# Kernel optimization log

Hardware: AMD Instinct MI355X
Metric: run time of the kernel (lower is better)

The kernel has to match this reference:

```python
import jax, jax.numpy as jnp
import numpy as np

LATENT = 256
HEADS = 4
DIM_HEAD = 256            # dim_head = latent_channels
INNER = HEADS * DIM_HEAD  # 1024
ROT_DIM = DIM_HEAD // 2   # rotary dim per coordinate (relative_emb_dim=2)
MIN_FREQ = 1.0 / 64.0     # 1/res
ROT_SCALE = 16.0          # CrossFormer scale
FF_SCALE = 0.5            # Gaussian Fourier feature scale
PI = 3.141592653589793
OUT_CH = 3


def _gelu(x):
    return jax.nn.gelu(x, approximate=False)  # torch nn.GELU default (erf)


def _rot_freqs(coords, dim):
    # coords: [b, n] -> freqs [b, n, dim]
    inv_freq = 1.0 / (10000.0 ** (jnp.arange(0, dim, 2, dtype=jnp.float32) / dim))
    t = coords * (ROT_SCALE / MIN_FREQ)
    f = t[..., None] * inv_freq               # [b, n, dim//2]
    return jnp.concatenate([f, f], axis=-1)    # [b, n, dim]


def _rotate_half(x):
    x1, x2 = jnp.split(x, 2, axis=-1)
    return jnp.concatenate([-x2, x1], axis=-1)


def _apply_rot(t, freqs):
    return t * jnp.cos(freqs) + _rotate_half(t) * jnp.sin(freqs)


def _apply_2d_rot(t, fx, fy):
    d = t.shape[-1]
    tx, ty = t[..., : d // 2], t[..., d // 2 :]
    return jnp.concatenate([_apply_rot(tx, fx), _apply_rot(ty, fy)], axis=-1)


def _inst_norm(t, eps=1e-5):
    # galerkin normalization: non-affine norm over head dim (InstanceNorm1d, affine=False)
    mu = jnp.mean(t, axis=-1, keepdims=True)
    var = jnp.var(t, axis=-1, keepdims=True)
    return (t - mu) * jax.lax.rsqrt(var + eps)


def setup_inputs() -> dict:
    key = jax.random.key(0)
    ks = jax.random.split(key, 20)
    b, nq, nc = 8, 4096, 4096
    s = 0.02
    return {
        "z": jax.random.normal(ks[0], (b, nc, LATENT), jnp.float32),
        "query_pos": jax.random.uniform(ks[1], (b, nq, 2), jnp.float32),
        "context_pos": jax.random.uniform(ks[2], (b, nc, 2), jnp.float32),
        # GaussianFourierFeatureTransform buffer B: [2, mapping_size=latent/2]
        "B_ff": jax.random.normal(ks[3], (2, LATENT // 2), jnp.float32) * FF_SCALE,
        # coordinate_projection linears (bias=False)
        "Wc1": jax.random.normal(ks[4], (LATENT, LATENT), jnp.float32) * s,
        "Wc2": jax.random.normal(ks[5], (LATENT, LATENT), jnp.float32) * s,
        # cross attention projections
        "Wq": jax.random.normal(ks[6], (LATENT, INNER), jnp.float32) * s,
        "Wkv": jax.random.normal(ks[7], (LATENT, 2 * INNER), jnp.float32) * s,
        "Wo": jax.random.normal(ks[8], (INNER, LATENT), jnp.float32) * s,
        "bo": jnp.zeros((LATENT,), jnp.float32),
        # feed-forward (mlp_dim = latent)
        "Wf1": jax.random.normal(ks[9], (LATENT, LATENT), jnp.float32) * s,
        "bf1": jnp.zeros((LATENT,), jnp.float32),
        "Wf2": jax.random.normal(ks[10], (LATENT, LATENT), jnp.float32) * s,
        "bf2": jnp.zeros((LATENT,), jnp.float32),
        # output head
        "Wh1": jax.random.normal(ks[11], (LATENT + 2, LATENT), jnp.float32) * s,
        "Wh2": jax.random.normal(ks[12], (LATENT, LATENT // 2), jnp.float32) * s,
        "Wh3": jax.random.normal(ks[13], (LATENT // 2, OUT_CH), jnp.float32) * s,
        "bh3": jnp.zeros((OUT_CH,), jnp.float32),
    }


def reference(z, query_pos, context_pos, B_ff, Wc1, Wc2, Wq, Wkv, Wo, bo,
              Wf1, bf1, Wf2, bf2, Wh1, Wh2, Wh3, bh3):
    b, nq, _ = query_pos.shape
    nc = z.shape[1]
    # 1) Gaussian Fourier features + 2-layer projection
    ff = 2.0 * PI * (query_pos @ B_ff)                           # [b, nq, latent/2]
    x = jnp.concatenate([jnp.sin(ff), jnp.cos(ff)], axis=-1)      # [b, nq, latent]
    x = _gelu(x @ Wc1) @ Wc2
    # 2) galerkin cross attention with 2D rotary relative pos emb
    q = (x @ Wq).reshape(b, nq, HEADS, DIM_HEAD).transpose(0, 2, 1, 3)
    k, v = jnp.split(z @ Wkv, 2, axis=-1)
    k = k.reshape(b, nc, HEADS, DIM_HEAD).transpose(0, 2, 1, 3)
    v = v.reshape(b, nc, HEADS, DIM_HEAD).transpose(0, 2, 1, 3)
    fxq = _rot_freqs(query_pos[..., 0], ROT_DIM)[:, None]         # [b,1,nq,rot]
    fyq = _rot_freqs(query_pos[..., 1], ROT_DIM)[:, None]
    fxk = _rot_freqs(context_pos[..., 0], ROT_DIM)[:, None]
    fyk = _rot_freqs(context_pos[..., 1], ROT_DIM)[:, None]
    q = _apply_2d_rot(q, fxq, fyq)
    k = _apply_2d_rot(k, fxk, fyk)
    k = _inst_norm(k)
    v = _inst_norm(v)
    kv = jnp.einsum('bhnd,bhne->bhde', k, v)                      # [b,h,d,d]
    attn = jnp.einsum('bhmd,bhde->bhme', q, kv) * (1.0 / nc)      # [b,h,nq,d]
    attn = attn.transpose(0, 2, 1, 3).reshape(b, nq, INNER)
    x = (attn @ Wo + bo) + x                                      # residual
    x = (_gelu(x @ Wf1 + bf1) @ Wf2 + bf2) + x                    # FFN residual
    # 3) output head on [features, coords]
    h = jnp.concatenate([x, query_pos], axis=-1)
    h = _gelu(h @ Wh1)
    h = _gelu(h @ Wh2)
    return h @ Wh3 + bh3                                          # [b, nq, out_ch]
```

## Files before the change

kernel.cpp:

```cpp
#include <hip/hip_runtime.h>
#include <math.h>


typedef unsigned short u16;
typedef __attribute__((ext_vector_type(4))) float f32x4;
typedef __attribute__((ext_vector_type(8))) short s16x8;
typedef __attribute__((ext_vector_type(8))) unsigned short u16x8;
typedef __attribute__((ext_vector_type(4))) unsigned short u16x4;

#define LOG2_1E4_D64 0.20762050593046013f

__device__ __forceinline__ u16 f2b(float f){
  union { float f; unsigned u; } v; v.f = f;
  unsigned u = v.u;
  u += 0x7FFFu + ((u >> 16) & 1u);
  return (u16)(u >> 16);
}
__device__ __forceinline__ float b2f(u16 b){
  union { unsigned u; float f; } v; v.u = ((unsigned)b) << 16; return v.f;
}
__device__ __forceinline__ float gelu_f(float x){
  return 0.5f * x * (1.0f + erff(x * 0.7071067811865475f));
}

#if __has_builtin(__builtin_amdgcn_global_load_lds)
#define HAVE_GLL 1
typedef const __attribute__((address_space(1))) void* as1cv;
typedef __attribute__((address_space(3))) void* as3v;
__device__ __forceinline__ void gload16(const void* g, void* l){
  __builtin_amdgcn_global_load_lds((as1cv)g, (as3v)l, 16, 0, 0);
}
#else
#define HAVE_GLL 0
#endif


__global__ __launch_bounds__(256) void k_cast(const float* __restrict__ in, u16* __restrict__ out){
  long i = (long)blockIdx.x * 256 + threadIdx.x;
  float4 f = ((const float4*)in)[i];
  u16x4 o = { f2b(f.x), f2b(f.y), f2b(f.z), f2b(f.w) };
  ((u16x4*)out)[i] = o;
}

struct TCArgs {
  const float* W[9]; u16* Wt[9];
  int K[9]; int N[9]; int boff[10];
};
__global__ __launch_bounds__(256) void k_tcast_all(TCArgs a){
  int b = blockIdx.x;
  int w = 0;
  while (b >= a.boff[w+1]) w++;
  int idx = (b - a.boff[w]) * 256 + threadIdx.x;
  int K = a.K[w], N = a.N[w];
  int n = idx / K, k = idx - n * K;
  a.Wt[w][idx] = f2b(a.W[w][(long)k * N + n]);
}

__global__ __launch_bounds__(256) void k_fourier(const float* __restrict__ qp, const float* __restrict__ Bff, u16* __restrict__ X0){
  int tid = threadIdx.x;
  long r = (long)blockIdx.x * 2 + (tid >> 7);
  int j = tid & 127;
  float qx = qp[r*2], qy = qp[r*2+1];
  float ff = 6.283185307179586f * (qx * Bff[j] + qy * Bff[128 + j]);
  X0[r*256 + j]       = f2b(sinf(ff));
  X0[r*256 + 128 + j] = f2b(cosf(ff));
}

__global__ __launch_bounds__(256) void k_red(const float* __restrict__ p, u16* __restrict__ out, long stride){
  long i = (long)blockIdx.x * 256 + threadIdx.x;
  f32x4 s = ((const f32x4*)p)[i];
  s += ((const f32x4*)(p + stride))[i];
  s += ((const f32x4*)(p + 2*stride))[i];
  s += ((const f32x4*)(p + 3*stride))[i];
  u16x4 o = { f2b(s[0]), f2b(s[1]), f2b(s[2]), f2b(s[3]) };
  ((u16x4*)out)[i] = o;
}

__global__ __launch_bounds__(256) void k_final(const u16* __restrict__ H2, const float* __restrict__ Wh3,
                                               const float* __restrict__ bh3, float* __restrict__ out){
  long r = (long)blockIdx.x * 256 + threadIdx.x;
  float a0 = bh3[0], a1 = bh3[1], a2 = bh3[2];
  const u16x8* hrow = (const u16x8*)(H2 + r*128);
#pragma unroll
  for (int c8 = 0; c8 < 16; c8++){
    u16x8 hv = hrow[c8];
#pragma unroll
    for (int e = 0; e < 8; e++){
      float f = b2f(hv[e]);
      int k = c8*8 + e;
      a0 += f * Wh3[k*3];
      a1 += f * Wh3[k*3+1];
      a2 += f * Wh3[k*3+2];
    }
  }
  out[r*3] = a0; out[r*3+1] = a1; out[r*3+2] = a2;
}


template<int MODE>
__global__ __launch_bounds__(256, 2)
void gemm_fuse(const u16* __restrict__ A, const u16* __restrict__ Bw,
               u16* __restrict__ out, const float* __restrict__ pos){
  __shared__ u16 As[128*32];
  __shared__ u16 Bs[256*32];

  int tid  = threadIdx.x;
  int lane = tid & 63;
  int wave = tid >> 6;
  int wm = (wave & 1) << 6;
  int wn = (wave >> 1) << 7;
  int whalf = wave >> 1;
  int h = blockIdx.y;
  long m0 = (long)blockIdx.x * 128;

  int r15 = lane & 15;
  int cc  = lane >> 4;
  const u16* Bh = Bw + (long)h * 65536;

#if HAVE_GLL
  int srow = lane >> 2;
  int scol = (lane & 3) * 8;
  u16* lA[2]; const u16* gA[2];
#pragma unroll
  for (int t = 0; t < 2; t++){
    int rb = (wave*2 + t) * 16;
    lA[t] = &As[rb*32];
    gA[t] = A + (m0 + rb + srow) * 256 + scol;
  }
  u16* lB[4]; const u16* gB[4];
#pragma unroll
  for (int t = 0; t < 4; t++){
    int rb = (wave*4 + t) * 16;
    lB[t] = &Bs[rb*32];
    gB[t] = Bh + (rb + srow) * 256 + scol;
  }
#else
  int sm  = tid >> 2;
  int sc  = tid & 3;
#endif

  f32x4 acc[4][8];
#pragma unroll
  for (int i = 0; i < 4; i++)
#pragma unroll
    for (int j = 0; j < 8; j++)
      acc[i][j] = f32x4{0.f, 0.f, 0.f, 0.f};

  for (int k0 = 0; k0 < 256; k0 += 32){
#if HAVE_GLL
    __syncthreads();
#pragma unroll
    for (int t = 0; t < 2; t++) gload16(gA[t] + k0, lA[t]);
#pragma unroll
    for (int t = 0; t < 4; t++) gload16(gB[t] + k0, lB[t]);
    __syncthreads();
#else
    u16x8 va = *(const u16x8*)(A + (m0 + sm)*256 + sc*8 + k0);
    u16x8 vb0 = *(const u16x8*)(Bh + (sm      )*256 + sc*8 + k0);
    u16x8 vb1 = *(const u16x8*)(Bh + (sm + 64 )*256 + sc*8 + k0);
    u16x8 vb2 = *(const u16x8*)(Bh + (sm + 128)*256 + sc*8 + k0);
    u16x8 vb3 = *(const u16x8*)(Bh + (sm + 192)*256 + sc*8 + k0);
    u16x8 va1 = *(const u16x8*)(A + (m0 + sm + 64)*256 + sc*8 + k0);
    __syncthreads();
    *(u16x8*)&As[sm*32 + sc*8] = va;
    *(u16x8*)&As[(sm+64)*32 + sc*8] = va1;
    *(u16x8*)&Bs[sm*32 + sc*8] = vb0;
    *(u16x8*)&Bs[(sm+64)*32 + sc*8] = vb1;
    *(u16x8*)&Bs[(sm+128)*32 + sc*8] = vb2;
    *(u16x8*)&Bs[(sm+192)*32 + sc*8] = vb3;
    __syncthreads();
#endif
    s16x8 af[4], bf[8];
#pragma unroll
    for (int i = 0; i < 4; i++) af[i] = *(const s16x8*)&As[(wm + i*16 + r15)*32 + cc*8];
#pragma unroll
    for (int j = 0; j < 8; j++) bf[j] = *(const s16x8*)&Bs[(wn + j*16 + r15)*32 + cc*8];
#pragma unroll
    for (int i = 0; i < 4; i++)
#pragma unroll
      for (int j = 0; j < 8; j++)
        acc[i][j] = __builtin_amdgcn_mfma_f32_16x16x32_bf16(af[i], bf[j], acc[i][j], 0, 0, 0);
  }

  if constexpr (MODE != 1){
    float invf4[4];
#pragma unroll
    for (int jl = 0; jl < 4; jl++)
      invf4[jl] = 1024.0f * exp2f(-(float)(jl*16 + r15) * LOG2_1E4_D64);
#pragma unroll
    for (int i = 0; i < 4; i++){
#pragma unroll
      for (int r = 0; r < 4; r++){
        long n = m0 + wm + i*16 + cc*4 + r;
        float p = pos[n*2 + whalf];
#pragma unroll
        for (int jl = 0; jl < 4; jl++){
          float a = p * invf4[jl];
          float s = __sinf(a), c = __cosf(a);
          float t0 = acc[i][jl][r], t1 = acc[i][jl+4][r];
          acc[i][jl][r]   = t0*c - t1*s;
          acc[i][jl+4][r] = t1*c + t0*s;
        }
      }
    }
  }

  if constexpr (MODE == 2){
#pragma unroll
    for (int i = 0; i < 4; i++)
#pragma unroll
      for (int j = 0; j < 8; j++)
#pragma unroll
        for (int r = 0; r < 4; r++){
          long row = m0 + wm + i*16 + cc*4 + r;
          int col = h*256 + wn + j*16 + r15;
          out[row*1024 + col] = f2b(acc[i][j][r]);
        }
  } else {
    __shared__ float PS1[2][128];
    __shared__ float PS2[2][128];
    __shared__ u16 TB[64*256];

    float s1a[4][4], s2a[4][4];
#pragma unroll
    for (int i = 0; i < 4; i++){
#pragma unroll
      for (int r = 0; r < 4; r++){
        float s1 = 0.f, s2 = 0.f;
#pragma unroll
        for (int j = 0; j < 8; j++){
          float v = acc[i][j][r];
          s1 += v; s2 += v*v;
        }
#pragma unroll
        for (int m = 1; m < 16; m <<= 1){
          s1 += __shfl_xor(s1, m, 64);
          s2 += __shfl_xor(s2, m, 64);
        }
        s1a[i][r] = s1; s2a[i][r] = s2;
        int rowid = (wave&1)*64 + i*16 + cc*4 + r;
        if (r15 == 0){ PS1[whalf][rowid] = s1; PS2[whalf][rowid] = s2; }
      }
    }
    __syncthreads();
#pragma unroll
    for (int i = 0; i < 4; i++){
#pragma unroll
      for (int r = 0; r < 4; r++){
        int rowid = (wave&1)*64 + i*16 + cc*4 + r;
        float s1 = PS1[0][rowid] + PS1[1][rowid];
        float s2 = PS2[0][rowid] + PS2[1][rowid];
        float mu  = s1 * 0.00390625f;
        float var = s2 * 0.00390625f - mu*mu;
        float inv = 1.0f / sqrtf(var + 1e-5f);
#pragma unroll
        for (int j = 0; j < 8; j++)
          acc[i][j] = f32x4{ (acc[i][j][0+0]-0.f), acc[i][j][1], acc[i][j][2], acc[i][j][3] },
          acc[i][j][r] = (acc[i][j][r] - mu) * inv;
      }
    }
    __syncthreads();

    int bb  = (int)(m0 >> 12);
    int nn0 = (int)(m0 & 4095);
    long matbase = ((long)(bb*4 + h) * 256) * 4096;
#pragma unroll
    for (int p = 0; p < 2; p++){
      if ((wave & 1) == p){
#pragma unroll
        for (int i = 0; i < 4; i++)
#pragma unroll
          for (int j = 0; j < 8; j++)
#pragma unroll
            for (int r = 0; r < 4; r++){
              int nl = i*16 + cc*4 + r;
              int d  = wn + j*16 + r15;
              TB[nl*256 + (d ^ ((nl>>2)<<1))] = f2b(acc[i][j][r]);
            }
      }
      __syncthreads();
      {
        int n4 = (lane & 15) * 4;
        int sw = (lane & 15) << 1;
#pragma unroll
        for (int rnd = 0; rnd < 16; rnd++){
          int d = rnd*16 + wave*4 + (lane >> 4);
          u16x4 vv;
#pragma unroll
          for (int jj = 0; jj < 4; jj++) vv[jj] = TB[(n4+jj)*256 + (d ^ sw)];
          *(u16x4*)(out + matbase + (long)d*4096 + nn0 + p*64 + n4) = vv;
        }
      }
      __syncthreads();
    }
  }
}


enum { EP_B = 0, EP_GELU = 1, EP_BIAS_GELU = 2, EP_BIAS_RESB = 3, EP_SCALE = 4,
       EP_QP_GELU = 5, EP_F32 = 6 };

struct GArgs {
  const u16* A; const u16* B;
  u16* Cb; float* Cf;
  const float* bias; const u16* res; const float* qp; const float* wtail;
  float scale;
  int M, N, K, lda, ldb, ldc, NLO;
  long sAh, sAl, sBh, sBl, sCh, sCl;
};

template<int EP>
__global__ __launch_bounds__(256, 2)
void gemm_k(GArgs g){
  int z = blockIdx.z;
  int zh = z / g.NLO, zl = z - zh * g.NLO;
  const u16* A = g.A + (long)zh * g.sAh + (long)zl * g.sAl;
  const u16* B = g.B + (long)zh * g.sBh + (long)zl * g.sBl;
  long coff = (long)zh * g.sCh + (long)zl * g.sCl;

  __shared__ u16 As[128*32];
  __shared__ u16 Bs[128*32];

  int tid  = threadIdx.x;
  int lane = tid & 63;
  int wave = tid >> 6;
  int wm = (wave & 1) << 6;
  int wn = (wave >> 1) << 6;
  long m0 = (long)blockIdx.x * 128;
  long n0 = (long)blockIdx.y * 128;

  int r15 = lane & 15;
  int cc  = lane >> 4;

#if HAVE_GLL
  int rA0 = (wave*2 + 0) * 16;
  int rA1 = (wave*2 + 1) * 16;
  int srow = lane >> 2;
  int scol = (lane & 3) * 8;
  u16* lA0 = &As[rA0*32];
  u16* lA1 = &As[rA1*32];
  u16* lB0 = &Bs[rA0*32];
  u16* lB1 = &Bs[rA1*32];
  const u16* gA0 = A + (m0 + rA0 + srow) * g.lda + scol;
  const u16* gA1 = A + (m0 + rA1 + srow) * g.lda + scol;
  const u16* gB0 = B + (n0 + rA0 + srow) * g.ldb + scol;
  const u16* gB1 = B + (n0 + rA1 + srow) * g.ldb + scol;
#else
  int sm  = tid >> 2;
  int sc  = tid & 3;
  int so0 = sm * 32 + sc * 8;
  int so1 = (sm + 64) * 32 + sc * 8;
  const u16* pA0 = A + (m0 + sm ) * g.lda + sc * 8;
  const u16* pA1 = A + (m0 + sm + 64) * g.lda + sc * 8;
  const u16* pB0 = B + (n0 + sm ) * g.ldb + sc * 8;
  const u16* pB1 = B + (n0 + sm + 64) * g.ldb + sc * 8;
#endif

  f32x4 acc[4][4];
#pragma unroll
  for (int i = 0; i < 4; i++)
#pragma unroll
    for (int j = 0; j < 4; j++)
      acc[i][j] = f32x4{0.f, 0.f, 0.f, 0.f};

  for (int k0 = 0; k0 < g.K; k0 += 32){
#if HAVE_GLL
    __syncthreads();
    gload16(gA0 + k0, lA0);
    gload16(gA1 + k0, lA1);
    gload16(gB0 + k0, lB0);
    gload16(gB1 + k0, lB1);
    __syncthreads();
#else
    u16x8 va0 = *(const u16x8*)(pA0 + k0);
    u16x8 va1 = *(const u16x8*)(pA1 + k0);
    u16x8 vb0 = *(const u16x8*)(pB0 + k0);
    u16x8 vb1 = *(const u16x8*)(pB1 + k0);
    __syncthreads();
    *(u16x8*)&As[so0] = va0;
    *(u16x8*)&As[so1] = va1;
    *(u16x8*)&Bs[so0] = vb0;
    *(u16x8*)&Bs[so1] = vb1;
    __syncthreads();
#endif
    s16x8 af[4], bf[4];
#pragma unroll
    for (int i = 0; i < 4; i++) af[i] = *(const s16x8*)&As[(wm + i*16 + r15)*32 + cc*8];
#pragma unroll
    for (int i = 0; i < 4; i++) bf[i] = *(const s16x8*)&Bs[(wn + i*16 + r15)*32 + cc*8];
#pragma unroll
    for (int i = 0; i < 4; i++)
#pragma unroll
      for (int j = 0; j < 4; j++)
        acc[i][j] = __builtin_amdgcn_mfma_f32_16x16x32_bf16(af[i], bf[j], acc[i][j], 0, 0, 0);
  }

  int colb = (int)n0 + wn + r15;
  int rowb = (int)m0 + wm + cc * 4;
#pragma unroll
  for (int i = 0; i < 4; i++){
#pragma unroll
    for (int j = 0; j < 4; j++){
      int col = colb + j*16;
#pragma unroll
      for (int r = 0; r < 4; r++){
        int row = rowb + i*16 + r;
        float v = acc[i][j][r];
        if constexpr (EP == EP_B){
          g.Cb[coff + (long)row * g.ldc + col] = f2b(v);
        } else if constexpr (EP == EP_GELU){
          g.Cb[coff + (long)row * g.ldc + col] = f2b(gelu_f(v));
        } else if constexpr (EP == EP_BIAS_GELU){
          v = gelu_f(v + g.bias[col]);
          g.Cb[coff + (long)row * g.ldc + col] = f2b(v);
        } else if constexpr (EP == EP_BIAS_RESB){
          v += g.bias[col] + b2f(g.res[(long)row * g.ldc + col]);
          g.Cb[coff + (long)row * g.ldc + col] = f2b(v);
        } else if constexpr (EP == EP_SCALE){
          g.Cb[coff + (long)row * g.ldc + col] = f2b(v * g.scale);
        } else if constexpr (EP == EP_F32){
          g.Cf[coff + (long)row * g.ldc + col] = v;
        } else {
          v += g.qp[(long)row*2] * g.wtail[col] + g.qp[(long)row*2+1] * g.wtail[256+col];
          g.Cb[coff + (long)row * g.ldc + col] = f2b(gelu_f(v));
        }
      }
    }
  }
}


extern "C" void kernel_launch(void* const* d_in, const int* in_sizes, int n_in,
                              void* d_out, int out_size, void* d_ws, size_t ws_size,
                              hipStream_t stream){
  const float* z   = (const float*)d_in[0];
  const float* qp  = (const float*)d_in[1];
  const float* cp  = (const float*)d_in[2];
  const float* Bff = (const float*)d_in[3];
  const float* Wc1 = (const float*)d_in[4];
  const float* Wc2 = (const float*)d_in[5];
  const float* Wq  = (const float*)d_in[6];
  const float* Wkv = (const float*)d_in[7];
  const float* Wo  = (const float*)d_in[8];
  const float* bo  = (const float*)d_in[9];
  const float* Wf1 = (const float*)d_in[10];
  const float* bf1 = (const float*)d_in[11];
  const float* Wf2 = (const float*)d_in[12];
  const float* bf2 = (const float*)d_in[13];
  const float* Wh1 = (const float*)d_in[14];
  const float* Wh2 = (const float*)d_in[15];
  const float* Wh3 = (const float*)d_in[16];
  const float* bh3 = (const float*)d_in[17];
  float* out = (float*)d_out;
  (void)in_sizes; (void)n_in; (void)out_size;

  size_t mb = ws_size >> 20;
  int C;
  if      (mb >= 264) C = 1;
  else if (mb >= 168) C = 2;
  else if (mb >= 120) C = 4;
  else                C = 8;
  const int NB = 8 / C;
  const long R = (long)NB * 4096;

  char* ws = (char*)d_ws;
  const size_t MB = 1024*1024;
  u16* WqT  = (u16*)(ws + 0);
  u16* WkvT = (u16*)(ws + 512*1024);
  u16* WoT  = (u16*)(ws + 1536*1024);
  u16* Wc1T = (u16*)(ws + 2048*1024);
  u16* Wc2T = (u16*)(ws + (2048+128)*1024);
  u16* Wf1T = (u16*)(ws + (2048+256)*1024);
  u16* Wf2T = (u16*)(ws + (2048+384)*1024);
  u16* Wh1T = (u16*)(ws + (2048+512)*1024);
  u16* Wh2T = (u16*)(ws + (2048+640)*1024);
  u16* R1 = (u16*)(ws + 4*MB);
  u16* R2 = (u16*)(ws + 20*MB);
  u16* R3 = (u16*)(ws + 36*MB);
  u16* R4 = (u16*)(ws + 52*MB);
  u16* kvT = (u16*)(ws + 68*MB);
  u16* BIG1 = (u16*)(ws + 72*MB);
  u16* BIG2 = (u16*)((char*)BIG1 + (size_t)NB*8*MB);
  u16* BIG3 = (u16*)((char*)BIG2 + (size_t)NB*8*MB);

  u16* X0b = R1; u16* X2b = R1;
  u16* Tb  = R2; u16* H1b = R2;
  u16* Xb  = R3;
  u16* Zb  = R4; u16* H2b = R4;

  auto G = [&](int ep, const u16* A, const u16* B, u16* Cb, float* Cf,
               const float* bias, const u16* res, const float* qq, const float* wtail,
               float scale, int M, int N, int K, int lda, int ldb, int ldc,
               int nz, int NLO, long sAh, long sAl, long sBh, long sBl, long sCh, long sCl){
    GArgs g;
    g.A=A; g.B=B; g.Cb=Cb; g.Cf=Cf; g.bias=bias; g.res=res; g.qp=qq; g.wtail=wtail;
    g.scale=scale; g.M=M; g.N=N; g.K=K; g.lda=lda; g.ldb=ldb; g.ldc=ldc; g.NLO=NLO;
    g.sAh=sAh; g.sAl=sAl; g.sBh=sBh; g.sBl=sBl; g.sCh=sCh; g.sCl=sCl;
    dim3 gr(M/128, N/128, nz); dim3 bl(256);
    switch(ep){
      case EP_B:          gemm_k<EP_B><<<gr,bl,0,stream>>>(g); break;
      case EP_GELU:       gemm_k<EP_GELU><<<gr,bl,0,stream>>>(g); break;
      case EP_BIAS_GELU:  gemm_k<EP_BIAS_GELU><<<gr,bl,0,stream>>>(g); break;
      case EP_BIAS_RESB:  gemm_k<EP_BIAS_RESB><<<gr,bl,0,stream>>>(g); break;
      case EP_SCALE:      gemm_k<EP_SCALE><<<gr,bl,0,stream>>>(g); break;
      case EP_QP_GELU:    gemm_k<EP_QP_GELU><<<gr,bl,0,stream>>>(g); break;
      case EP_F32:        gemm_k<EP_F32><<<gr,bl,0,stream>>>(g); break;
    }
  };

  k_cast<<<dim3(8192), dim3(256), 0, stream>>>(z, Zb);
  {
    TCArgs a;
    const float* Ws[9] = { Wq, Wkv, Wo, Wc1, Wc2, Wf1, Wf2, Wh1, Wh2 };
    u16* Wts[9] = { WqT, WkvT, WoT, Wc1T, Wc2T, Wf1T, Wf2T, Wh1T, Wh2T };
    int Ks[9] = { 256, 256, 1024, 256, 256, 256, 256, 256, 256 };
    int Ns[9] = { 1024, 2048, 256, 256, 256, 256, 256, 256, 128 };
    int off = 0;
    for (int i = 0; i < 9; i++){
      a.W[i] = Ws[i]; a.Wt[i] = Wts[i]; a.K[i] = Ks[i]; a.N[i] = Ns[i];
      a.boff[i] = off; off += Ks[i]*Ns[i]/256;
    }
    a.boff[9] = off;
    k_tcast_all<<<dim3(off), dim3(256), 0, stream>>>(a);
  }

  k_fourier<<<dim3(16384), dim3(256), 0, stream>>>(qp, Bff, X0b);
  G(EP_GELU, X0b, Wc1T, Tb, 0, 0,0,0,0, 1.f, 32768,256,256, 256,256,256, 1,1, 0,0,0,0,0,0);
  G(EP_B,    Tb,  Wc2T, Xb, 0, 0,0,0,0, 1.f, 32768,256,256, 256,256,256, 1,1, 0,0,0,0,0,0);

  for (int c = 0; c < C; c++){
    long row0 = (long)c * R;
    const u16* Zc = Zb + row0 * 256;
    gemm_fuse<0><<<dim3((int)(R/128), 4), dim3(256), 0, stream>>>(Zc, WkvT, BIG2, cp + row0*2);
    gemm_fuse<1><<<dim3((int)(R/128), 4), dim3(256), 0, stream>>>(Zc, WkvT + 1024*256, BIG3, cp + row0*2);
    G(EP_F32, BIG3, BIG2, 0, (float*)BIG1, 0,0,0,0, 1.f,
      256,256,1024, 4096,4096,256, 4*NB*4, NB*4,
      1024,1048576, 1024,1048576, (long)NB*4*65536,65536);
    k_red<<<dim3(NB*256), dim3(256), 0, stream>>>((float*)BIG1, kvT + (long)c*NB*4*65536, (long)NB*4*65536);
    gemm_fuse<2><<<dim3((int)(R/128), 4), dim3(256), 0, stream>>>(Xb + row0*256, WqT, BIG1, qp + row0*2);
    G(EP_SCALE, BIG1, kvT + (long)c*NB*4*65536, BIG2, 0, 0,0,0,0, 1.0f/4096.0f,
      4096,256,256, 1024,256,1024, NB*4,4, 4194304,256, 262144,65536, 4194304,256);
    G(EP_BIAS_RESB, BIG2, WoT, X2b + row0*256, 0, bo, Xb + row0*256, 0,0, 1.f,
      (int)R,256,1024, 1024,1024,256, 1,1, 0,0,0,0,0,0);
  }

  G(EP_BIAS_GELU, X2b, Wf1T, Tb, 0, bf1, 0,0,0, 1.f, 32768,256,256, 256,256,256, 1,1, 0,0,0,0,0,0);
  G(EP_BIAS_RESB, Tb, Wf2T, Xb, 0, bf2, X2b, 0,0, 1.f, 32768,256,256, 256,256,256, 1,1, 0,0,0,0,0,0);
  G(EP_QP_GELU, Xb, Wh1T, H1b, 0, 0,0, qp, Wh1 + 65536, 1.f, 32768,256,256, 256,256,256, 1,1, 0,0,0,0,0,0);
  G(EP_GELU, H1b, Wh2T, H2b, 0, 0,0,0,0, 1.f, 32768,128,256, 256,256,128, 1,1, 0,0,0,0,0,0);
  k_final<<<dim3(128), dim3(256), 0, stream>>>(H2b, Wh3, bh3, out);
}
```

Before: 603.1 us.

## Double-buffer LDS tiles in GEMMs and merge K/V projection launches

Both the fused projection kernel and the generic GEMM now double-buffer their shared-memory tiles, prefetching the next K-slice with global-to-LDS loads while MFMAs run on the current one, which removes one barrier per iteration. The separate K and V projection launches are merged into one launch with 8 column blocks, using a block-index check to pick rotary and output target. The grid is reordered so column blocks vary fastest, for A-tile reuse in cache. Shared memory is reused through one 48KB buffer, which may limit occupancy, and the non-GLL fallback was rewritten awkwardly.

```diff
diff --git a/kernel.cpp b/kernel.cpp
--- a/kernel.cpp
+++ b/kernel.cpp
@@ -100,9 +100,11 @@
 template<int MODE>
 __global__ __launch_bounds__(256, 2)
 void gemm_fuse(const u16* __restrict__ A, const u16* __restrict__ Bw,
-               u16* __restrict__ out, const float* __restrict__ pos){
-  __shared__ u16 As[128*32];
-  __shared__ u16 Bs[256*32];
+               u16* __restrict__ outK, u16* __restrict__ outV,
+               const float* __restrict__ pos){
+  __shared__ char smem[49152];
+  u16* AsB[2] = { (u16*)smem,            (u16*)(smem + 8192)  };
+  u16* BsB[2] = { (u16*)(smem + 16384),  (u16*)(smem + 32768) };
 
   int tid  = threadIdx.x;
   int lane = tid & 63;
@@ -110,34 +112,29 @@
   int wm = (wave & 1) << 6;
   int wn = (wave >> 1) << 7;
   int whalf = wave >> 1;
-  int h = blockIdx.y;
-  long m0 = (long)blockIdx.x * 128;
+  int yb = blockIdx.x;
+  int h  = yb & 3;
+  bool isK = (MODE == 1) || (yb < 4);
+  long m0 = (long)blockIdx.y * 128;
 
   int r15 = lane & 15;
   int cc  = lane >> 4;
-  const u16* Bh = Bw + (long)h * 65536;
-
-#if HAVE_GLL
+  const u16* Bh = Bw + (long)yb * 65536;
+
   int srow = lane >> 2;
   int scol = (lane & 3) * 8;
-  u16* lA[2]; const u16* gA[2];
+  int aRow[2], bRow[4];
+  const u16 *gA[2], *gB[4];
 #pragma unroll
   for (int t = 0; t < 2; t++){
-    int rb = (wave*2 + t) * 16;
-    lA[t] = &As[rb*32];
-    gA[t] = A + (m0 + rb + srow) * 256 + scol;
-  }
-  u16* lB[4]; const u16* gB[4];
+    aRow[t] = (wave*2 + t) * 16;
+    gA[t] = A + (m0 + aRow[t] + srow) * 256 + scol;
+  }
 #pragma unroll
   for (int t = 0; t < 4; t++){
-    int rb = (wave*4 + t) * 16;
-    lB[t] = &Bs[rb*32];
-    gB[t] = Bh + (rb + srow) * 256 + scol;
-  }
-#else
-  int sm  = tid >> 2;
-  int sc  = tid & 3;
-#endif
+    bRow[t] = (wave*4 + t) * 16;
+    gB[t] = Bh + (bRow[t] + srow) * 256 + scol;
+  }
 
   f32x4 acc[4][8];
 #pragma unroll
@@ -146,43 +143,70 @@
     for (int j = 0; j < 8; j++)
       acc[i][j] = f32x4{0.f, 0.f, 0.f, 0.f};
 
+#if HAVE_GLL
+#pragma unroll
+  for (int t = 0; t < 2; t++) gload16(gA[t], AsB[0] + aRow[t]*32);
+#pragma unroll
+  for (int t = 0; t < 4; t++) gload16(gB[t], BsB[0] + bRow[t]*32);
+  __syncthreads();
+  int cur = 0;
   for (int k0 = 0; k0 < 256; k0 += 32){
-#if HAVE_GLL
-    __syncthreads();
-#pragma unroll
-    for (int t = 0; t < 2; t++) gload16(gA[t] + k0, lA[t]);
-#pragma unroll
-    for (int t = 0; t < 4; t++) gload16(gB[t] + k0, lB[t]);
-    __syncthreads();
+    int nxt = cur ^ 1;
+    if (k0 < 224){
+#pragma unroll
+      for (int t = 0; t < 2; t++) gload16(gA[t] + k0 + 32, AsB[nxt] + aRow[t]*32);
+#pragma unroll
+      for (int t = 0; t < 4; t++) gload16(gB[t] + k0 + 32, BsB[nxt] + bRow[t]*32);
+    }
+    s16x8 af[4], bf[8];
+#pragma unroll
+    for (int i = 0; i < 4; i++) af[i] = *(const s16x8*)&AsB[cur][(wm + i*16 + r15)*32 + cc*8];
+#pragma unroll
+    for (int j = 0; j < 8; j++) bf[j] = *(const s16x8*)&BsB[cur][(wn + j*16 + r15)*32 + cc*8];
+#pragma unroll
+    for (int i = 0; i < 4; i++)
+#pragma unroll
+      for (int j = 0; j < 8; j++)
+        acc[i][j] = __builtin_amdgcn_mfma_f32_16x16x32_bf16(af[i], bf[j], acc[i][j], 0, 0, 0);
+    __syncthreads();
+    cur = nxt;
+  }
 #else
-    u16x8 va = *(const u16x8*)(A + (m0 + sm)*256 + sc*8 + k0);
+  int sm = tid >> 2, sc = tid & 3;
+  for (int k0 = 0; k0 < 256; k0 += 32){
+    u16x8 va  = *(const u16x8*)(A + (m0 + sm)*256 + sc*8 + k0);
+    u16x8 va1 = *(const u16x8*)(A + (m0 + sm + 64)*256 + sc*8 + k0);
     u16x8 vb0 = *(const u16x8*)(Bh + (sm      )*256 + sc*8 + k0);
     u16x8 vb1 = *(const u16x8*)(Bh + (sm + 64 )*256 + sc*8 + k0);
     u16x8 vb2 = *(const u16x8*)(Bh + (sm + 128)*256 + sc*8 + k0);
     u16x8 vb3 = *(const u16x8*)(Bh + (sm + 192)*256 + sc*8 + k0);
-    u16x8 va1 = *(const u16x8*)(A + (m0 + sm + 64)*256 + sc*8 + k0);
-    __syncthreads();
-    *(u16x8*)&As[sm*32 + sc*8] = va;
-    *(u16x8*)&As[(sm+64)*32 + sc*8] = va1;
-    *(u16x8*)&Bs[sm*32 + sc*8] = vb0;
-    *(u16x8*)&Bs[(sm+64)*32 + sc*8] = vb1;
-    *(u16x8*)&Bs[(sm+128)*32 + sc*8] = vb2;
-    *(u16x8*)&Bs[(sm+192)*32 + sc*8] = vb3;
-    __syncthreads();
-#endif
+    __syncthreads();
+    *(u16x8*)&AsB[0][sm*32 + sc*8] = va;
+    *(u16x8*)&AsB[0][(sm+64)*32 + sc*8] = va1;
+    *(u16x8*)&BsB[0][sm*32 + sc*8] = vb0;
+    *(u16x8*)&BsB[0][(sm+64)*32 + sc*8] = vb1;
+    *(u16x8*)&BsB[1][sm*32 + sc*8] = vb2;
+    *(u16x8*)&BsB[1][(sm+64)*32 + sc*8] = vb3;
+    __syncthreads();
     s16x8 af[4], bf[8];
 #pragma unroll
-    for (int i = 0; i < 4; i++) af[i] = *(const s16x8*)&As[(wm + i*16 + r15)*32 + cc*8];
-#pragma unroll
-    for (int j = 0; j < 8; j++) bf[j] = *(const s16x8*)&Bs[(wn + j*16 + r15)*32 + cc*8];
+    for (int i = 0; i < 4; i++) af[i] = *(const s16x8*)&AsB[0][(wm + i*16 + r15)*32 + cc*8];
+#pragma unroll
+    for (int j = 0; j < 8; j++){
+      int rr = wn + j*16 + r15;
+      bf[j] = (rr < 128) ? *(const s16x8*)&BsB[0][rr*32 + cc*8]
+                         : *(const s16x8*)&BsB[1][(rr-128)*32 + cc*8];
+    }
 #pragma unroll
     for (int i = 0; i < 4; i++)
 #pragma unroll
       for (int j = 0; j < 8; j++)
         acc[i][j] = __builtin_amdgcn_mfma_f32_16x16x32_bf16(af[i], bf[j], acc[i][j], 0, 0, 0);
-  }
-
-  if constexpr (MODE != 1){
+    __syncthreads();
+  }
+#endif
+
+  if (isK){
     float invf4[4];
 #pragma unroll
     for (int jl = 0; jl < 4; jl++)
@@ -205,7 +229,7 @@
     }
   }
 
-  if constexpr (MODE == 2){
+  if constexpr (MODE == 1){
 #pragma unroll
     for (int i = 0; i < 4; i++)
 #pragma unroll
@@ -213,15 +237,14 @@
 #pragma unroll
         for (int r = 0; r < 4; r++){
           long row = m0 + wm + i*16 + cc*4 + r;
-          int col = h*256 + wn + j*16 + r15;
-          out[row*1024 + col] = f2b(acc[i][j][r]);
+          int col = yb*256 + wn + j*16 + r15;
+          outK[row*1024 + col] = f2b(acc[i][j][r]);
         }
   } else {
-    __shared__ float PS1[2][128];
-    __shared__ float PS2[2][128];
-    __shared__ u16 TB[64*256];
-
-    float s1a[4][4], s2a[4][4];
+    u16*   TB  = (u16*)smem;
+    float* PS1 = (float*)(smem + 32768);
+    float* PS2 = (float*)(smem + 33792);
+
 #pragma unroll
     for (int i = 0; i < 4; i++){
 #pragma unroll
@@ -237,9 +260,8 @@
           s1 += __shfl_xor(s1, m, 64);
           s2 += __shfl_xor(s2, m, 64);
         }
-        s1a[i][r] = s1; s2a[i][r] = s2;
         int rowid = (wave&1)*64 + i*16 + cc*4 + r;
-        if (r15 == 0){ PS1[whalf][rowid] = s1; PS2[whalf][rowid] = s2; }
+        if (r15 == 0){ PS1[whalf*128 + rowid] = s1; PS2[whalf*128 + rowid] = s2; }
       }
     }
     __syncthreads();
@@ -248,19 +270,19 @@
 #pragma unroll
       for (int r = 0; r < 4; r++){
         int rowid = (wave&1)*64 + i*16 + cc*4 + r;
-        float s1 = PS1[0][rowid] + PS1[1][rowid];
-        float s2 = PS2[0][rowid] + PS2[1][rowid];
+        float s1 = PS1[rowid] + PS1[128 + rowid];
+        float s2 = PS2[rowid] + PS2[128 + rowid];
         float mu  = s1 * 0.00390625f;
         float var = s2 * 0.00390625f - mu*mu;
         float inv = 1.0f / sqrtf(var + 1e-5f);
 #pragma unroll
         for (int j = 0; j < 8; j++)
-          acc[i][j] = f32x4{ (acc[i][j][0+0]-0.f), acc[i][j][1], acc[i][j][2], acc[i][j][3] },
           acc[i][j][r] = (acc[i][j][r] - mu) * inv;
       }
     }
     __syncthreads();
 
+    u16* outp = isK ? outK : outV;
     int bb  = (int)(m0 >> 12);
     int nn0 = (int)(m0 & 4095);
     long matbase = ((long)(bb*4 + h) * 256) * 4096;
@@ -288,7 +310,7 @@
           u16x4 vv;
 #pragma unroll
           for (int jj = 0; jj < 4; jj++) vv[jj] = TB[(n4+jj)*256 + (d ^ sw)];
-          *(u16x4*)(out + matbase + (long)d*4096 + nn0 + p*64 + n4) = vv;
+          *(u16x4*)(outp + matbase + (long)d*4096 + nn0 + p*64 + n4) = vv;
         }
       }
       __syncthreads();
@@ -318,8 +340,8 @@
   const u16* B = g.B + (long)zh * g.sBh + (long)zl * g.sBl;
   long coff = (long)zh * g.sCh + (long)zl * g.sCl;
 
-  __shared__ u16 As[128*32];
-  __shared__ u16 Bs[128*32];
+  __shared__ u16 As[2][128*32];
+  __shared__ u16 Bs[2][128*32];
 
   int tid  = threadIdx.x;
   int lane = tid & 63;
@@ -332,68 +354,77 @@
   int r15 = lane & 15;
   int cc  = lane >> 4;
 
+  f32x4 acc[4][4];
+#pragma unroll
+  for (int i = 0; i < 4; i++)
+#pragma unroll
+    for (int j = 0; j < 4; j++)
+      acc[i][j] = f32x4{0.f, 0.f, 0.f, 0.f};
+
 #if HAVE_GLL
-  int rA0 = (wave*2 + 0) * 16;
-  int rA1 = (wave*2 + 1) * 16;
   int srow = lane >> 2;
   int scol = (lane & 3) * 8;
-  u16* lA0 = &As[rA0*32];
-  u16* lA1 = &As[rA1*32];
-  u16* lB0 = &Bs[rA0*32];
-  u16* lB1 = &Bs[rA1*32];
-  const u16* gA0 = A + (m0 + rA0 + srow) * g.lda + scol;
-  const u16* gA1 = A + (m0 + rA1 + srow) * g.lda + scol;
-  const u16* gB0 = B + (n0 + rA0 + srow) * g.ldb + scol;
-  const u16* gB1 = B + (n0 + rA1 + srow) * g.ldb + scol;
+  int aRow[2];
+  const u16 *gA[2], *gB[2];
+#pragma unroll
+  for (int t = 0; t < 2; t++){
+    aRow[t] = (wave*2 + t) * 16;
+    gA[t] = A + (m0 + aRow[t] + srow) * g.lda + scol;
+    gB[t] = B + (n0 + aRow[t] + srow) * g.ldb + scol;
+  }
+#pragma unroll
+  for (int t = 0; t < 2; t++){ gload16(gA[t], As[0] + aRow[t]*32); gload16(gB[t], Bs[0] + aRow[t]*32); }
+  __syncthreads();
+  int cur = 0;
+  for (int k0 = 0; k0 < g.K; k0 += 32){
+    int nxt = cur ^ 1;
+    if (k0 + 32 < g.K){
+#pragma unroll
+      for (int t = 0; t < 2; t++){
+        gload16(gA[t] + k0 + 32, As[nxt] + aRow[t]*32);
+        gload16(gB[t] + k0 + 32, Bs[nxt] + aRow[t]*32);
+      }
+    }
+    s16x8 af[4], bf[4];
+#pragma unroll
+    for (int i = 0; i < 4; i++) af[i] = *(const s16x8*)&As[cur][(wm + i*16 + r15)*32 + cc*8];
+#pragma unroll
+    for (int i = 0; i < 4; i++) bf[i] = *(const s16x8*)&Bs[cur][(wn + i*16 + r15)*32 + cc*8];
+#pragma unroll
+    for (int i = 0; i < 4; i++)
+#pragma unroll
+      for (int j = 0; j < 4; j++)
+        acc[i][j] = __builtin_amdgcn_mfma_f32_16x16x32_bf16(af[i], bf[j], acc[i][j], 0, 0, 0);
+    __syncthreads();
+    cur = nxt;
+  }
 #else
   int sm  = tid >> 2;
   int sc  = tid & 3;
-  int so0 = sm * 32 + sc * 8;
-  int so1 = (sm + 64) * 32 + sc * 8;
-  const u16* pA0 = A + (m0 + sm ) * g.lda + sc * 8;
-  const u16* pA1 = A + (m0 + sm + 64) * g.lda + sc * 8;
-  const u16* pB0 = B + (n0 + sm ) * g.ldb + sc * 8;
-  const u16* pB1 = B + (n0 + sm + 64) * g.ldb + sc * 8;
-#endif
-
-  f32x4 acc[4][4];
-#pragma unroll
-  for (int i = 0; i < 4; i++)
-#pragma unroll
-    for (int j = 0; j < 4; j++)
-      acc[i][j] = f32x4{0.f, 0.f, 0.f, 0.f};
-
   for (int k0 = 0; k0 < g.K; k0 += 32){
-#if HAVE_GLL
-    __syncthreads();
-    gload16(gA0 + k0, lA0);
-    gload16(gA1 + k0, lA1);
-    gload16(gB0 + k0, lB0);
-    gload16(gB1 + k0, lB1);
-    __syncthreads();
-#else
-    u16x8 va0 = *(const u16x8*)(pA0 + k0);
-    u16x8 va1 = *(const u16x8*)(pA1 + k0);
-    u16x8 vb0 = *(const u16x8*)(pB0 + k0);
-    u16x8 vb1 = *(const u16x8*)(pB1 + k0);
-    __syncthreads();
-    *(u16x8*)&As[so0] = va0;
-    *(u16x8*)&As[so1] = va1;
-    *(u16x8*)&Bs[so0] = vb0;
-    *(u16x8*)&Bs[so1] = vb1;
-    __syncthreads();
-#endif
+    u16x8 va0 = *(const u16x8*)(A + (m0 + sm )*g.lda + sc*8 + k0);
+    u16x8 va1 = *(const u16x8*)(A + (m0 + sm + 64)*g.lda + sc*8 + k0);
+    u16x8 vb0 = *(const u16x8*)(B + (n0 + sm )*g.ldb + sc*8 + k0);
+    u16x8 vb1 = *(const u16x8*)(B + (n0 + sm + 64)*g.ldb + sc*8 + k0);
+    __syncthreads();
+    *(u16x8*)&As[0][sm*32 + sc*8] = va0;
+    *(u16x8*)&As[0][(sm+64)*32 + sc*8] = va1;
+    *(u16x8*)&Bs[0][sm*32 + sc*8] = vb0;
+    *(u16x8*)&Bs[0][(sm+64)*32 + sc*8] = vb1;
+    __syncthreads();
     s16x8 af[4], bf[4];
 #pragma unroll
-    for (int i = 0; i < 4; i++) af[i] = *(const s16x8*)&As[(wm + i*16 + r15)*32 + cc*8];
-#pragma unroll
-    for (int i = 0; i < 4; i++) bf[i] = *(const s16x8*)&Bs[(wn + i*16 + r15)*32 + cc*8];
+    for (int i = 0; i < 4; i++) af[i] = *(const s16x8*)&As[0][(wm + i*16 + r15)*32 + cc*8];
+#pragma unroll
+    for (int i = 0; i < 4; i++) bf[i] = *(const s16x8*)&Bs[0][(wn + i*16 + r15)*32 + cc*8];
 #pragma unroll
     for (int i = 0; i < 4; i++)
 #pragma unroll
       for (int j = 0; j < 4; j++)
         acc[i][j] = __builtin_amdgcn_mfma_f32_16x16x32_bf16(af[i], bf[j], acc[i][j], 0, 0, 0);
-  }
+    __syncthreads();
+  }
+#endif
 
   int colb = (int)n0 + wn + r15;
   int rowb = (int)m0 + wm + cc * 4;
@@ -531,13 +562,12 @@
   for (int c = 0; c < C; c++){
     long row0 = (long)c * R;
     const u16* Zc = Zb + row0 * 256;
-    gemm_fuse<0><<<dim3((int)(R/128), 4), dim3(256), 0, stream>>>(Zc, WkvT, BIG2, cp + row0*2);
-    gemm_fuse<1><<<dim3((int)(R/128), 4), dim3(256), 0, stream>>>(Zc, WkvT + 1024*256, BIG3, cp + row0*2);
+    gemm_fuse<0><<<dim3(8, (int)(R/128)), dim3(256), 0, stream>>>(Zc, WkvT, BIG2, BIG3, cp + row0*2);
     G(EP_F32, BIG3, BIG2, 0, (float*)BIG1, 0,0,0,0, 1.f,
       256,256,1024, 4096,4096,256, 4*NB*4, NB*4,
       1024,1048576, 1024,1048576, (long)NB*4*65536,65536);
     k_red<<<dim3(NB*256), dim3(256), 0, stream>>>((float*)BIG1, kvT + (long)c*NB*4*65536, (long)NB*4*65536);
-    gemm_fuse<2><<<dim3((int)(R/128), 4), dim3(256), 0, stream>>>(Xb + row0*256, WqT, BIG1, qp + row0*2);
+    gemm_fuse<1><<<dim3(4, (int)(R/128)), dim3(256), 0, stream>>>(Xb + row0*256, WqT, BIG1, 0, qp + row0*2);
     G(EP_SCALE, BIG1, kvT + (long)c*NB*4*65536, BIG2, 0, 0,0,0,0, 1.0f/4096.0f,
       4096,256,256, 1024,256,1024, NB*4,4, 4194304,256, 262144,65536, 4194304,256);
     G(EP_BIAS_RESB, BIG2, WoT, X2b + row0*256, 0, bo, Xb + row0*256, 0,0, 1.f,
```

Result: faster. 540.4 us (-10.4%).
